# Performance work log

Measured on AMD Instinct MI355X. Metric: run time of the kernel, lower is better.

Reference implementation:

```python
import jax, jax.numpy as jnp
import numpy as np

# Convex_f forward. D and mid are fixed tridiagonal matrices:
#   (D x)[i]   = -x[i-1] + 2*x[i] - x[i+1]  for 1 <= i <= n-2, and 0 at i=0, n-1
#   (mid x)[i] = 0.5*(x[i-1] + x[i+1])      for 1 <= i <= n-2,
#                0.5*x[1] at i=0, 0.5*x[n-2] at i=n-1
# We implement these as direct 3-point stencils (same math as the dense matmuls).

B, N, K = 256, 8192, 16

def setup_inputs() -> dict:
    key = jax.random.key(0)
    k1, k2 = jax.random.split(key)
    x = jax.random.normal(k1, (B, N, K), dtype=jnp.float32)
    param = jax.random.normal(k2, (B, N, K), dtype=jnp.float32)
    return {"x": x, "param": param}

def _convex_step(y):
    # y: [B, N, K]
    up, ctr, dn = y[:, :-2], y[:, 1:-1], y[:, 2:]
    Dy_in = -up + 2.0 * ctr - dn                      # interior rows of D @ y
    Dy = jnp.pad(Dy_in, ((0, 0), (1, 1), (0, 0)))     # rows 0 and N-1 zeroed
    mid_y = jnp.concatenate(
        [0.5 * y[:, 1:2], 0.5 * (up + dn), 0.5 * y[:, -2:-1]], axis=1
    )                                                 # mid @ y
    dy = (Dy > 0).astype(y.dtype) * (y - mid_y)
    return y - dy

def reference(x, param):
    y = x + param
    return _convex_step(y) - param
```

## Files before the change

kernel.cpp:

```cpp
#include <hip/hip_runtime.h>


typedef float f32x4 __attribute__((ext_vector_type(4)));

#define B_      256
#define N_      8192
#define KQ      4
#define R_      8
#define GROUPS  64
#define TILE    (GROUPS * R_)
#define TILES_N (N_ / TILE)

__global__ __launch_bounds__(256)
void convex_kernel(const f32x4* __restrict__ x4,
                   const f32x4* __restrict__ p4,
                   f32x4* __restrict__ o4)
{
    const int tid = threadIdx.x;
    const int g   = tid >> 2;
    const int c   = tid & 3;
    const int t   = blockIdx.x & (TILES_N - 1);
    const int b   = blockIdx.x >> 4;
    const int n0  = t * TILE + g * R_;
    const long rowbase = (long)b * N_;

    f32x4 xv[R_ + 2], pv[R_ + 2];
#pragma unroll
    for (int j = 0; j < R_ + 2; ++j) {
        int row = n0 - 1 + j;
        row = row < 0 ? 0 : row;
        row = row > N_ - 1 ? N_ - 1 : row;
        const long idx = (rowbase + row) * KQ + c;
        xv[j] = x4[idx];
        pv[j] = p4[idx];
    }

#pragma unroll
    for (int j = 0; j < R_; ++j) {
        const int n = n0 + j;
        f32x4 r;
        if (n == 0 || n == N_ - 1) {
            r = xv[j + 1];
        } else {
            const f32x4 ym = xv[j]     + pv[j];
            const f32x4 yc = xv[j + 1] + pv[j + 1];
            const f32x4 yp = xv[j + 2] + pv[j + 2];
            const f32x4 m  = 0.5f * (ym + yp);
            f32x4 mn;
            mn.x = fminf(yc.x, m.x);
            mn.y = fminf(yc.y, m.y);
            mn.z = fminf(yc.z, m.z);
            mn.w = fminf(yc.w, m.w);
            r = mn - pv[j + 1];
        }
        __builtin_nontemporal_store(r, &o4[(rowbase + n) * KQ + c]);
    }
}

extern "C" void kernel_launch(void* const* d_in, const int* in_sizes, int n_in,
                              void* d_out, int out_size, void* d_ws, size_t ws_size,
                              hipStream_t stream)
{
    const f32x4* x = (const f32x4*)d_in[0];
    const f32x4* p = (const f32x4*)d_in[1];
    f32x4*       o = (f32x4*)d_out;

    dim3 grid(B_ * TILES_N);
    dim3 block(256);
    convex_kernel<<<grid, block, 0, stream>>>(x, p, o);
}
```

Baseline: 326.3 us.

## Stream rows per wave and share stencil neighbours via lane shuffles

Each wave now walks a 256-row span in chunks of 16 rows, loading each row of x and param once. Neighbour rows come from cross-lane shuffles, with the previous and next chunk carried in registers. This removes the redundant halo loads of the per-thread 10-row window. The cost is a serial dependency chain with only one chunk of prefetch, which lowers memory-level parallelism per wave and adds shuffle instructions.

After: 323.3 us. No clear change (-0.9%).

```diff
diff --git a/kernel.cpp b/kernel.cpp
--- a/kernel.cpp
+++ b/kernel.cpp
@@ -3,57 +3,97 @@
 
 typedef float f32x4 __attribute__((ext_vector_type(4)));
 
-#define B_      256
-#define N_      8192
-#define KQ      4
-#define R_      8
-#define GROUPS  64
-#define TILE    (GROUPS * R_)
-#define TILES_N (N_ / TILE)
+#define B_    256
+#define N_    8192
+#define KQ    4
+#define CH    16
+#define SPAN  256
+#define M_    (SPAN / CH)
+#define WPB   4
+#define SPB   (N_ / SPAN)
+
+__device__ __forceinline__ f32x4 shfl4(f32x4 v, int src) {
+    f32x4 r;
+    r.x = __shfl(v.x, src);
+    r.y = __shfl(v.y, src);
+    r.z = __shfl(v.z, src);
+    r.w = __shfl(v.w, src);
+    return r;
+}
 
 __global__ __launch_bounds__(256)
 void convex_kernel(const f32x4* __restrict__ x4,
                    const f32x4* __restrict__ p4,
                    f32x4* __restrict__ o4)
 {
-    const int tid = threadIdx.x;
-    const int g   = tid >> 2;
-    const int c   = tid & 3;
-    const int t   = blockIdx.x & (TILES_N - 1);
-    const int b   = blockIdx.x >> 4;
-    const int n0  = t * TILE + g * R_;
-    const long rowbase = (long)b * N_;
+    const int tid  = threadIdx.x;
+    const int lane = tid & 63;
+    const int wv   = tid >> 6;
+    const int gw   = blockIdx.x * WPB + wv;
+    const int b    = gw >> 5;
+    const int s    = (gw & 31) * SPAN;
+    const int lr   = lane >> 2;
+    const int c    = lane & 3;
 
-    f32x4 xv[R_ + 2], pv[R_ + 2];
-#pragma unroll
-    for (int j = 0; j < R_ + 2; ++j) {
-        int row = n0 - 1 + j;
-        row = row < 0 ? 0 : row;
-        row = row > N_ - 1 ? N_ - 1 : row;
-        const long idx = (rowbase + row) * KQ + c;
-        xv[j] = x4[idx];
-        pv[j] = p4[idx];
+    const long batch = (long)b * N_ * KQ;
+
+    const int rup = (s - 1 < 0) ? 0 : s - 1;
+    const int rdn = (s + SPAN > N_ - 1) ? N_ - 1 : s + SPAN;
+    f32x4 y_prev, y_edge_dn;
+    {
+        long i = batch + (long)rup * KQ + c;
+        y_prev = x4[i] + p4[i];
+    }
+    {
+        long i = batch + (long)rdn * KQ + c;
+        y_edge_dn = x4[i] + p4[i];
     }
 
-#pragma unroll
-    for (int j = 0; j < R_; ++j) {
-        const int n = n0 + j;
-        f32x4 r;
-        if (n == 0 || n == N_ - 1) {
-            r = xv[j + 1];
+    long idx = batch + (long)(s + lr) * KQ + c;
+    f32x4 p_c = p4[idx];
+    f32x4 y_cur = x4[idx] + p_c;
+
+    const int idx_up = (lane + 60) & 63;
+    const int idx_dn = (lane + 4) & 63;
+    const bool lo = (lane < 4);
+    const bool hi = (lane >= 60);
+
+    f32x4 p_n = p_c, y_next;
+
+#pragma unroll 2
+    for (int j = 0; j < M_; ++j) {
+        if (j < M_ - 1) {
+            const long ni = idx + CH * KQ;
+            f32x4 xn = x4[ni];
+            p_n = p4[ni];
+            y_next = xn + p_n;
         } else {
-            const f32x4 ym = xv[j]     + pv[j];
-            const f32x4 yc = xv[j + 1] + pv[j + 1];
-            const f32x4 yp = xv[j + 2] + pv[j + 2];
-            const f32x4 m  = 0.5f * (ym + yp);
-            f32x4 mn;
-            mn.x = fminf(yc.x, m.x);
-            mn.y = fminf(yc.y, m.y);
-            mn.z = fminf(yc.z, m.z);
-            mn.w = fminf(yc.w, m.w);
-            r = mn - pv[j + 1];
+            y_next = y_edge_dn;
         }
-        __builtin_nontemporal_store(r, &o4[(rowbase + n) * KQ + c]);
+
+        const f32x4 up_c = shfl4(y_cur,  idx_up);
+        const f32x4 up_p = shfl4(y_prev, idx_up);
+        const f32x4 dn_c = shfl4(y_cur,  idx_dn);
+        const f32x4 dn_n = shfl4(y_next, idx_dn);
+        const f32x4 up = lo ? up_p : up_c;
+        const f32x4 dn = hi ? dn_n : dn_c;
+
+        const f32x4 mid = 0.5f * (up + dn);
+        f32x4 mn;
+        mn.x = fminf(y_cur.x, mid.x);
+        mn.y = fminf(y_cur.y, mid.y);
+        mn.z = fminf(y_cur.z, mid.z);
+        mn.w = fminf(y_cur.w, mid.w);
+
+        const int n = s + j * CH + lr;
+        if (n == 0 || n == N_ - 1) mn = y_cur;
+
+        __builtin_nontemporal_store(mn - p_c, &o4[idx]);
+
+        y_prev = y_cur;
+        y_cur  = y_next;
+        p_c    = p_n;
+        idx   += CH * KQ;
     }
 }
 
@@ -65,7 +105,7 @@
     const f32x4* p = (const f32x4*)d_in[1];
     f32x4*       o = (f32x4*)d_out;
 
-    dim3 grid(B_ * TILES_N);
+    dim3 grid(B_ * SPB / WPB);
     dim3 block(256);
     convex_kernel<<<grid, block, 0, stream>>>(x, p, o);
 }
```
